# Kernel optimization log

Measured on AMD Instinct MI355X. Metric: run time of the kernel, lower is better.

## Reference

```python
import jax, jax.numpy as jnp
import numpy as np

L = 3        # num_layers
B = 8192     # batch slots
H = 1024     # hidden_dim (== decoder_in_dim)
D_IN = 1024
D_OUT = 80
N_ACT = 4096 # active rows selected by hidden_idx


def setup_inputs() -> dict:
    key = jax.random.key(0)
    ks = jax.random.split(key, 8)
    encoded = jax.random.normal(ks[0], (B, D_IN), jnp.float32)
    hidden = jax.random.normal(ks[1], (L, B, H), jnp.float32)
    hidden_idx = jnp.arange(N_ACT, dtype=jnp.int32)  # unique, in-range batch indices
    s = 0.05  # small init scale for stable gate math
    w_ih = jax.random.normal(ks[2], (L, 3 * H, D_IN), jnp.float32) * s
    w_hh = jax.random.normal(ks[3], (L, 3 * H, H), jnp.float32) * s
    b_ih = jax.random.normal(ks[4], (L, 3 * H), jnp.float32) * s
    b_hh = jax.random.normal(ks[5], (L, 3 * H), jnp.float32) * s
    w_out = jax.random.normal(ks[6], (D_OUT, H), jnp.float32) * s
    b_out = jax.random.normal(ks[7], (D_OUT,), jnp.float32) * s
    return {"encoded": encoded, "hidden": hidden, "hidden_idx": hidden_idx,
            "w_ih": w_ih, "w_hh": w_hh, "b_ih": b_ih, "b_hh": b_hh,
            "w_out": w_out, "b_out": b_out}


def reference(encoded, hidden, hidden_idx, w_ih, w_hh, b_ih, b_hh, w_out, b_out):
    # Gather active rows, run stacked GRUCells, scatter back (eval mode: dropout = identity).
    x = encoded[hidden_idx]                       # [N, D_IN]
    new_hidden = []
    for i in range(L):                            # small fixed layer loop
        h_full = hidden[i]                        # [B, H]
        h = h_full[hidden_idx]                    # [N, H]
        gi = x @ w_ih[i].T + b_ih[i]              # [N, 3H] gates from input
        gh = h @ w_hh[i].T + b_hh[i]              # [N, 3H] gates from hidden
        i_r, i_z, i_n = jnp.split(gi, 3, axis=-1)
        h_r, h_z, h_n = jnp.split(gh, 3, axis=-1)
        r = jax.nn.sigmoid(i_r + h_r)
        z = jax.nn.sigmoid(i_z + h_z)
        n = jnp.tanh(i_n + r * h_n)
        h_out = (1.0 - z) * n + z * h             # torch GRUCell update
        x = h_out
        new_hidden.append(h_full.at[hidden_idx].set(h_out))
    y = jnp.tanh(x @ w_out.T + b_out)             # linear head + tanh activation
    output = jnp.zeros((B, D_OUT), y.dtype).at[hidden_idx].set(y)
    return (output, jnp.stack(new_hidden))
```

## Files before the change

kernel.cpp:

```cpp
#include <hip/hip_runtime.h>

typedef unsigned short ushort_t;
typedef unsigned int uint_t;
typedef __attribute__((ext_vector_type(8))) short bf16x8;
typedef __attribute__((ext_vector_type(4))) float f32x4;

constexpr int L_   = 3;
constexpr int B_   = 8192;
constexpr int H_   = 1024;
constexpr int DIN_ = 1024;
constexpr int DOUT_= 80;
constexpr int NACT_= 4096;
constexpr int G3_  = 3 * H_;

static __device__ __forceinline__ ushort_t f2bf(float f) {
    uint_t u = __float_as_uint(f);
    uint_t r = (u + 0x7FFFu + ((u >> 16) & 1u)) >> 16;
    return (ushort_t)r;
}

static __device__ __forceinline__ void gll16(const void* g, void* l) {
    __builtin_amdgcn_global_load_lds(
        (const __attribute__((address_space(1))) uint32_t*)g,
        (__attribute__((address_space(3))) uint32_t*)l, 16, 0, 0);
}

__global__ void prep_convert(const float* __restrict__ wih, const float* __restrict__ whh,
                             const float* __restrict__ wout,
                             ushort_t* __restrict__ oih, ushort_t* __restrict__ ohh,
                             ushort_t* __restrict__ oout) {
    int tid = blockIdx.x * blockDim.x + threadIdx.x;
    int nth = gridDim.x * blockDim.x;
    const int NW = L_ * G3_ * H_ / 4;
    for (int i = tid; i < NW; i += nth) {
        float4 a = ((const float4*)wih)[i];
        ushort4 o; o.x = f2bf(a.x); o.y = f2bf(a.y); o.z = f2bf(a.z); o.w = f2bf(a.w);
        ((ushort4*)oih)[i] = o;
        float4 b = ((const float4*)whh)[i];
        ushort4 p; p.x = f2bf(b.x); p.y = f2bf(b.y); p.z = f2bf(b.z); p.w = f2bf(b.w);
        ((ushort4*)ohh)[i] = p;
    }
    const int NO = DOUT_ * H_ / 4;
    for (int i = tid; i < NO; i += nth) {
        float4 a = ((const float4*)wout)[i];
        ushort4 o; o.x = f2bf(a.x); o.y = f2bf(a.y); o.z = f2bf(a.z); o.w = f2bf(a.w);
        ((ushort4*)oout)[i] = o;
    }
}

__global__ void prep_gather(const float* __restrict__ encoded, const float* __restrict__ hidden,
                            const int* __restrict__ idx,
                            ushort_t* __restrict__ x0, ushort_t* __restrict__ hb) {
    const int C4 = H_ / 4;
    const int PER = NACT_ * C4;
    int tid = blockIdx.x * blockDim.x + threadIdx.x;
    int nth = gridDim.x * blockDim.x;
    int total = 4 * PER;
    for (int i = tid; i < total; i += nth) {
        int seg = i / PER;
        int rem = i - seg * PER;
        int r = rem / C4, c = rem % C4;
        int gr = idx[r];
        const float* src = (seg == 0) ? (encoded + (size_t)gr * DIN_)
                                      : (hidden + ((size_t)(seg - 1) * B_ + gr) * H_);
        float4 v = ((const float4*)src)[c];
        ushort4 o; o.x = f2bf(v.x); o.y = f2bf(v.y); o.z = f2bf(v.z); o.w = f2bf(v.w);
        ushort_t* dst = (seg == 0) ? x0 : (hb + (size_t)(seg - 1) * NACT_ * H_);
        ((ushort4*)(dst + (size_t)r * H_))[c] = o;
    }
}

__global__ __launch_bounds__(256, 2) void gru_layer(
    const ushort_t* __restrict__ xb,
    const ushort_t* __restrict__ hb,
    const float* __restrict__ hid_full,
    const ushort_t* __restrict__ wih,
    const ushort_t* __restrict__ whh,
    const float* __restrict__ bih, const float* __restrict__ bhh,
    const int* __restrict__ idx,
    float* __restrict__ out_hid,
    ushort_t* __restrict__ xnext)
{
    __shared__ ushort_t As[128 * 64];
    __shared__ ushort_t Ws[192 * 64];

    const int tid = threadIdx.x;
    const int bid = blockIdx.x;
    const int swz = (bid & 7) * 64 + (bid >> 3);
    const int bn = swz & 15, bm = swz >> 4;
    const int row0 = bm * 128, col0 = bn * 64;
    const int wave = tid >> 6, lane = tid & 63;
    const int wr = wave >> 1, wc = wave & 1;
    const int fl = lane & 15, fh = lane >> 4;
    const int srow = lane >> 3;
    const int sxor = ((lane & 7) ^ srow) * 8;

    f32x4 accR[4][2] = {};
    f32x4 accZ[4][2] = {};
    f32x4 accN[2][4][2] = {};

#pragma unroll
    for (int ph = 0; ph < 2; ++ph) {
        const ushort_t* Asrc = ph ? hb : xb;
        const ushort_t* Wsrc = ph ? whh : wih;
        const ushort_t* abase[4];
        const ushort_t* wbase[6];
#pragma unroll
        for (int t = 0; t < 4; ++t)
            abase[t] = Asrc + (size_t)(row0 + wave * 32 + t * 8 + srow) * H_ + sxor;
#pragma unroll
        for (int t = 0; t < 6; ++t) {
            const int slot = wave * 48 + t * 8 + srow;
            const int gate = slot >> 6, rowW = slot & 63;
            wbase[t] = Wsrc + (size_t)(gate * H_ + col0 + rowW) * H_ + sxor;
        }
        for (int kk = 0; kk < H_; kk += 64) {
            __syncthreads();
#pragma unroll
            for (int t = 0; t < 4; ++t)
                gll16(abase[t] + kk, &As[wave * 2048 + t * 512]);
#pragma unroll
            for (int t = 0; t < 6; ++t)
                gll16(wbase[t] + kk, &Ws[wave * 3072 + t * 512]);
            __syncthreads();
#pragma unroll
            for (int ks = 0; ks < 2; ++ks) {
                const int sl = ((ks * 4 + fh) ^ (fl & 7)) * 8;
                bf16x8 a[4];
#pragma unroll
                for (int m = 0; m < 4; ++m)
                    a[m] = *(const bf16x8*)&As[(wr * 64 + m * 16 + fl) * 64 + sl];
#pragma unroll
                for (int g = 0; g < 3; ++g) {
#pragma unroll
                    for (int n = 0; n < 2; ++n) {
                        const bf16x8 b = *(const bf16x8*)&Ws[(g * 64 + wc * 32 + n * 16 + fl) * 64 + sl];
#pragma unroll
                        for (int m = 0; m < 4; ++m) {
                            if (g == 0)
                                accR[m][n] = __builtin_amdgcn_mfma_f32_16x16x32_bf16(a[m], b, accR[m][n], 0, 0, 0);
                            else if (g == 1)
                                accZ[m][n] = __builtin_amdgcn_mfma_f32_16x16x32_bf16(a[m], b, accZ[m][n], 0, 0, 0);
                            else
                                accN[ph][m][n] = __builtin_amdgcn_mfma_f32_16x16x32_bf16(a[m], b, accN[ph][m][n], 0, 0, 0);
                        }
                    }
                }
            }
        }
    }

#pragma unroll
    for (int m = 0; m < 4; ++m) {
#pragma unroll
        for (int n = 0; n < 2; ++n) {
            const int c = col0 + wc * 32 + n * 16 + fl;
            const float br_r = bih[c] + bhh[c];
            const float br_z = bih[H_ + c] + bhh[H_ + c];
            const float bi_n = bih[2 * H_ + c];
            const float bh_n = bhh[2 * H_ + c];
#pragma unroll
            for (int j = 0; j < 4; ++j) {
                const int r = row0 + wr * 64 + m * 16 + fh * 4 + j;
                const float vr = 1.f / (1.f + expf(-(accR[m][n][j] + br_r)));
                const float vz = 1.f / (1.f + expf(-(accZ[m][n][j] + br_z)));
                const float vn = tanhf(accN[0][m][n][j] + bi_n + vr * (accN[1][m][n][j] + bh_n));
                const int gr = idx[r];
                const float h0 = hid_full[(size_t)gr * H_ + c];
                const float ho = (1.f - vz) * vn + vz * h0;
                out_hid[(size_t)gr * H_ + c] = ho;
                xnext[(size_t)r * H_ + c] = f2bf(ho);
            }
        }
    }
}

__global__ __launch_bounds__(256) void head_gemm(
    const ushort_t* __restrict__ xb, const ushort_t* __restrict__ wo,
    const float* __restrict__ bo, const int* __restrict__ idx,
    float* __restrict__ outy)
{
    __shared__ ushort_t Xs[64][72];
    __shared__ ushort_t Ws[80][72];
    const int tid = threadIdx.x;
    const int row0 = blockIdx.x * 64;
    const int lrow = tid >> 2, lseg = tid & 3;
    const int wave = tid >> 6, lane = tid & 63;
    const int fl = lane & 15, fh = lane >> 4;
    f32x4 acc[5] = {};

    for (int kk = 0; kk < H_; kk += 64) {
        __syncthreads();
        const ushort_t* xp = xb + (size_t)(row0 + lrow) * H_ + kk + lseg * 16;
        *(uint4*)&Xs[lrow][lseg * 16]     = *(const uint4*)xp;
        *(uint4*)&Xs[lrow][lseg * 16 + 8] = *(const uint4*)(xp + 8);
        for (int t = tid; t < 320; t += 256) {
            int r = t >> 2, s = t & 3;
            const ushort_t* wp = wo + (size_t)r * H_ + kk + s * 16;
            *(uint4*)&Ws[r][s * 16]     = *(const uint4*)wp;
            *(uint4*)&Ws[r][s * 16 + 8] = *(const uint4*)(wp + 8);
        }
        __syncthreads();
#pragma unroll
        for (int ks = 0; ks < 64; ks += 32) {
            bf16x8 a = *(const bf16x8*)&Xs[wave * 16 + fl][ks + fh * 8];
#pragma unroll
            for (int nf = 0; nf < 5; ++nf) {
                bf16x8 b = *(const bf16x8*)&Ws[nf * 16 + fl][ks + fh * 8];
                acc[nf] = __builtin_amdgcn_mfma_f32_16x16x32_bf16(a, b, acc[nf], 0, 0, 0);
            }
        }
    }
#pragma unroll
    for (int nf = 0; nf < 5; ++nf) {
        const int c = nf * 16 + fl;
        const float bb = bo[c];
#pragma unroll
        for (int j = 0; j < 4; ++j) {
            const int r = row0 + wave * 16 + fh * 4 + j;
            const float y = tanhf(acc[nf][j] + bb);
            outy[(size_t)idx[r] * DOUT_ + c] = y;
        }
    }
}

extern "C" void kernel_launch(void* const* d_in, const int* in_sizes, int n_in,
                              void* d_out, int out_size, void* d_ws, size_t ws_size,
                              hipStream_t stream) {
    const float* encoded = (const float*)d_in[0];
    const float* hidden  = (const float*)d_in[1];
    const int*   idx     = (const int*)d_in[2];
    const float* w_ih    = (const float*)d_in[3];
    const float* w_hh    = (const float*)d_in[4];
    const float* b_ih    = (const float*)d_in[5];
    const float* b_hh    = (const float*)d_in[6];
    const float* w_out   = (const float*)d_in[7];
    const float* b_out   = (const float*)d_in[8];

    float* outy = (float*)d_out;
    float* outh = outy + (size_t)B_ * DOUT_;

    ushort_t* ws    = (ushort_t*)d_ws;
    ushort_t* wihb  = ws;
    ushort_t* whhb  = wihb + (size_t)L_ * G3_ * H_;
    ushort_t* woutb = whhb + (size_t)L_ * G3_ * H_;
    ushort_t* xb0   = woutb + (size_t)DOUT_ * H_;
    ushort_t* xb1   = xb0 + (size_t)NACT_ * H_;
    ushort_t* hb    = xb1 + (size_t)NACT_ * H_;

    hipMemsetAsync(outy, 0, (size_t)B_ * DOUT_ * sizeof(float), stream);
    hipMemcpyAsync(outh, hidden, (size_t)L_ * B_ * H_ * sizeof(float),
                   hipMemcpyDeviceToDevice, stream);

    prep_convert<<<2048, 256, 0, stream>>>(w_ih, w_hh, w_out, wihb, whhb, woutb);
    prep_gather<<<2048, 256, 0, stream>>>(encoded, hidden, idx, xb0, hb);

    ushort_t* xin = xb0;
    ushort_t* xout = xb1;
    for (int i = 0; i < L_; ++i) {
        gru_layer<<<512, 256, 0, stream>>>(
            xin, hb + (size_t)i * NACT_ * H_, hidden + (size_t)i * B_ * H_,
            wihb + (size_t)i * G3_ * H_, whhb + (size_t)i * G3_ * H_,
            b_ih + (size_t)i * G3_, b_hh + (size_t)i * G3_, idx,
            outh + (size_t)i * B_ * H_, xout);
        ushort_t* t = xin; xin = xout; xout = t;
    }
    head_gemm<<<64, 256, 0, stream>>>(xin, woutb, b_out, idx, outy);
}
```

Before: 289.1 us.

## Use 32x32 MFMA tiles, fuse prep kernels, copy only inactive hidden rows

Switches the GRU layer GEMM from 16x16x32 to 32x32x16 bf16 MFMA, which cuts LDS fragment reads per MFMA. The two prep kernels are merged into one launch that also builds a mask of active rows. The full device-to-device hidden-state copy is replaced by a masked copy inside each layer kernel, so only inactive rows are copied. This removes redundant writes of active rows and one launch, at the cost of a mask memset and a byte lookup per copied element.

Measured after the change: 324.3 us. 12.2% more time.

```diff
diff --git a/kernel.cpp b/kernel.cpp
--- a/kernel.cpp
+++ b/kernel.cpp
@@ -1,14 +1,14 @@
 #include <hip/hip_runtime.h>
 
 typedef unsigned short ushort_t;
+typedef unsigned char uchar_t;
 typedef unsigned int uint_t;
 typedef __attribute__((ext_vector_type(8))) short bf16x8;
-typedef __attribute__((ext_vector_type(4))) float f32x4;
+typedef __attribute__((ext_vector_type(16))) float f32x16;
 
 constexpr int L_   = 3;
 constexpr int B_   = 8192;
 constexpr int H_   = 1024;
-constexpr int DIN_ = 1024;
 constexpr int DOUT_= 80;
 constexpr int NACT_= 4096;
 constexpr int G3_  = 3 * H_;
@@ -25,12 +25,19 @@
         (__attribute__((address_space(3))) uint32_t*)l, 16, 0, 0);
 }
 
-__global__ void prep_convert(const float* __restrict__ wih, const float* __restrict__ whh,
-                             const float* __restrict__ wout,
-                             ushort_t* __restrict__ oih, ushort_t* __restrict__ ohh,
-                             ushort_t* __restrict__ oout) {
+#define MFMA32(A, B, C) __builtin_amdgcn_mfma_f32_32x32x16_bf16((A), (B), (C), 0, 0, 0)
+
+__global__ void prep_all(const float* __restrict__ encoded, const float* __restrict__ hidden,
+                         const int* __restrict__ idx,
+                         const float* __restrict__ wih, const float* __restrict__ whh,
+                         const float* __restrict__ wout,
+                         ushort_t* __restrict__ oih, ushort_t* __restrict__ ohh,
+                         ushort_t* __restrict__ oout,
+                         ushort_t* __restrict__ x0, ushort_t* __restrict__ hb,
+                         uchar_t* __restrict__ mask) {
     int tid = blockIdx.x * blockDim.x + threadIdx.x;
     int nth = gridDim.x * blockDim.x;
+    if (tid < NACT_) mask[idx[tid]] = 1;
     const int NW = L_ * G3_ * H_ / 4;
     for (int i = tid; i < NW; i += nth) {
         float4 a = ((const float4*)wih)[i];
@@ -46,22 +53,14 @@
         ushort4 o; o.x = f2bf(a.x); o.y = f2bf(a.y); o.z = f2bf(a.z); o.w = f2bf(a.w);
         ((ushort4*)oout)[i] = o;
     }
-}
-
-__global__ void prep_gather(const float* __restrict__ encoded, const float* __restrict__ hidden,
-                            const int* __restrict__ idx,
-                            ushort_t* __restrict__ x0, ushort_t* __restrict__ hb) {
     const int C4 = H_ / 4;
     const int PER = NACT_ * C4;
-    int tid = blockIdx.x * blockDim.x + threadIdx.x;
-    int nth = gridDim.x * blockDim.x;
-    int total = 4 * PER;
-    for (int i = tid; i < total; i += nth) {
+    for (int i = tid; i < 4 * PER; i += nth) {
         int seg = i / PER;
         int rem = i - seg * PER;
         int r = rem / C4, c = rem % C4;
         int gr = idx[r];
-        const float* src = (seg == 0) ? (encoded + (size_t)gr * DIN_)
+        const float* src = (seg == 0) ? (encoded + (size_t)gr * H_)
                                       : (hidden + ((size_t)(seg - 1) * B_ + gr) * H_);
         float4 v = ((const float4*)src)[c];
         ushort4 o; o.x = f2bf(v.x); o.y = f2bf(v.y); o.z = f2bf(v.z); o.w = f2bf(v.w);
@@ -79,7 +78,8 @@
     const float* __restrict__ bih, const float* __restrict__ bhh,
     const int* __restrict__ idx,
     float* __restrict__ out_hid,
-    ushort_t* __restrict__ xnext)
+    ushort_t* __restrict__ xnext,
+    const uchar_t* __restrict__ mask)
 {
     __shared__ ushort_t As[128 * 64];
     __shared__ ushort_t Ws[192 * 64];
@@ -91,87 +91,75 @@
     const int row0 = bm * 128, col0 = bn * 64;
     const int wave = tid >> 6, lane = tid & 63;
     const int wr = wave >> 1, wc = wave & 1;
-    const int fl = lane & 15, fh = lane >> 4;
-    const int srow = lane >> 3;
-    const int sxor = ((lane & 7) ^ srow) * 8;
-
-    f32x4 accR[4][2] = {};
-    f32x4 accZ[4][2] = {};
-    f32x4 accN[2][4][2] = {};
+    const int l5 = lane & 31, hk = lane >> 5;
+    const int sr = lane >> 3, ss = (lane & 7) ^ sr;
+
+    f32x16 accR[2] = {}, accZ[2] = {}, accN[2][2] = {};
 
 #pragma unroll
     for (int ph = 0; ph < 2; ++ph) {
         const ushort_t* Asrc = ph ? hb : xb;
         const ushort_t* Wsrc = ph ? whh : wih;
-        const ushort_t* abase[4];
-        const ushort_t* wbase[6];
+        const ushort_t* ab[4];
+        const ushort_t* wb[6];
 #pragma unroll
         for (int t = 0; t < 4; ++t)
-            abase[t] = Asrc + (size_t)(row0 + wave * 32 + t * 8 + srow) * H_ + sxor;
+            ab[t] = Asrc + (size_t)(row0 + wave * 32 + t * 8 + sr) * H_ + ss * 8;
 #pragma unroll
         for (int t = 0; t < 6; ++t) {
-            const int slot = wave * 48 + t * 8 + srow;
-            const int gate = slot >> 6, rowW = slot & 63;
-            wbase[t] = Wsrc + (size_t)(gate * H_ + col0 + rowW) * H_ + sxor;
+            const int fr = wave * 48 + t * 8 + sr;
+            wb[t] = Wsrc + (size_t)((fr >> 6) * H_ + col0 + (fr & 63)) * H_ + ss * 8;
         }
         for (int kk = 0; kk < H_; kk += 64) {
             __syncthreads();
 #pragma unroll
-            for (int t = 0; t < 4; ++t)
-                gll16(abase[t] + kk, &As[wave * 2048 + t * 512]);
-#pragma unroll
-            for (int t = 0; t < 6; ++t)
-                gll16(wbase[t] + kk, &Ws[wave * 3072 + t * 512]);
+            for (int t = 0; t < 4; ++t) gll16(ab[t] + kk, &As[(wave * 32 + t * 8) * 64]);
+#pragma unroll
+            for (int t = 0; t < 6; ++t) gll16(wb[t] + kk, &Ws[(wave * 48 + t * 8) * 64]);
             __syncthreads();
 #pragma unroll
-            for (int ks = 0; ks < 2; ++ks) {
-                const int sl = ((ks * 4 + fh) ^ (fl & 7)) * 8;
-                bf16x8 a[4];
-#pragma unroll
-                for (int m = 0; m < 4; ++m)
-                    a[m] = *(const bf16x8*)&As[(wr * 64 + m * 16 + fl) * 64 + sl];
-#pragma unroll
-                for (int g = 0; g < 3; ++g) {
-#pragma unroll
-                    for (int n = 0; n < 2; ++n) {
-                        const bf16x8 b = *(const bf16x8*)&Ws[(g * 64 + wc * 32 + n * 16 + fl) * 64 + sl];
-#pragma unroll
-                        for (int m = 0; m < 4; ++m) {
-                            if (g == 0)
-                                accR[m][n] = __builtin_amdgcn_mfma_f32_16x16x32_bf16(a[m], b, accR[m][n], 0, 0, 0);
-                            else if (g == 1)
-                                accZ[m][n] = __builtin_amdgcn_mfma_f32_16x16x32_bf16(a[m], b, accZ[m][n], 0, 0, 0);
-                            else
-                                accN[ph][m][n] = __builtin_amdgcn_mfma_f32_16x16x32_bf16(a[m], b, accN[ph][m][n], 0, 0, 0);
-                        }
-                    }
-                }
+            for (int s = 0; s < 4; ++s) {
+                const int sl = (((s * 2 + hk) ^ (lane & 7)) << 3);
+                const bf16x8 a0 = *(const bf16x8*)&As[((wr * 64 + l5) << 6) + sl];
+                const bf16x8 a1 = *(const bf16x8*)&As[((wr * 64 + 32 + l5) << 6) + sl];
+                const bf16x8 b0 = *(const bf16x8*)&Ws[((wc * 32 + l5) << 6) + sl];
+                const bf16x8 b1 = *(const bf16x8*)&Ws[((64 + wc * 32 + l5) << 6) + sl];
+                const bf16x8 b2 = *(const bf16x8*)&Ws[((128 + wc * 32 + l5) << 6) + sl];
+                accR[0] = MFMA32(a0, b0, accR[0]);
+                accR[1] = MFMA32(a1, b0, accR[1]);
+                accZ[0] = MFMA32(a0, b1, accZ[0]);
+                accZ[1] = MFMA32(a1, b1, accZ[1]);
+                accN[ph][0] = MFMA32(a0, b2, accN[ph][0]);
+                accN[ph][1] = MFMA32(a1, b2, accN[ph][1]);
             }
         }
     }
 
-#pragma unroll
-    for (int m = 0; m < 4; ++m) {
-#pragma unroll
-        for (int n = 0; n < 2; ++n) {
-            const int c = col0 + wc * 32 + n * 16 + fl;
-            const float br_r = bih[c] + bhh[c];
-            const float br_z = bih[H_ + c] + bhh[H_ + c];
-            const float bi_n = bih[2 * H_ + c];
-            const float bh_n = bhh[2 * H_ + c];
-#pragma unroll
-            for (int j = 0; j < 4; ++j) {
-                const int r = row0 + wr * 64 + m * 16 + fh * 4 + j;
-                const float vr = 1.f / (1.f + expf(-(accR[m][n][j] + br_r)));
-                const float vz = 1.f / (1.f + expf(-(accZ[m][n][j] + br_z)));
-                const float vn = tanhf(accN[0][m][n][j] + bi_n + vr * (accN[1][m][n][j] + bh_n));
-                const int gr = idx[r];
-                const float h0 = hid_full[(size_t)gr * H_ + c];
-                const float ho = (1.f - vz) * vn + vz * h0;
-                out_hid[(size_t)gr * H_ + c] = ho;
-                xnext[(size_t)r * H_ + c] = f2bf(ho);
-            }
-        }
+    const int c = col0 + wc * 32 + l5;
+    const float br_r = bih[c] + bhh[c];
+    const float br_z = bih[H_ + c] + bhh[H_ + c];
+    const float bi_n = bih[2 * H_ + c];
+    const float bh_n = bhh[2 * H_ + c];
+#pragma unroll
+    for (int mf = 0; mf < 2; ++mf) {
+#pragma unroll
+        for (int reg = 0; reg < 16; ++reg) {
+            const int r = row0 + wr * 64 + mf * 32 + (reg & 3) + ((reg >> 2) << 3) + (hk << 2);
+            const float vr = 1.f / (1.f + expf(-(accR[mf][reg] + br_r)));
+            const float vz = 1.f / (1.f + expf(-(accZ[mf][reg] + br_z)));
+            const float vn = tanhf(accN[0][mf][reg] + bi_n + vr * (accN[1][mf][reg] + bh_n));
+            const int gr = idx[r];
+            const float h0 = hid_full[(size_t)gr * H_ + c];
+            const float ho = (1.f - vz) * vn + vz * h0;
+            out_hid[(size_t)gr * H_ + c] = ho;
+            xnext[(size_t)r * H_ + c] = f2bf(ho);
+        }
+    }
+
+    const int tot = B_ * (H_ / 4);
+    for (int i = bid * 256 + tid; i < tot; i += 512 * 256) {
+        const int row = i >> 8;
+        if (!mask[row]) ((float4*)out_hid)[i] = ((const float4*)hid_full)[i];
     }
 }
 
@@ -182,6 +170,7 @@
 {
     __shared__ ushort_t Xs[64][72];
     __shared__ ushort_t Ws[80][72];
+    typedef __attribute__((ext_vector_type(4))) float f32x4;
     const int tid = threadIdx.x;
     const int row0 = blockIdx.x * 64;
     const int lrow = tid >> 2, lseg = tid & 3;
@@ -247,13 +236,12 @@
     ushort_t* xb0   = woutb + (size_t)DOUT_ * H_;
     ushort_t* xb1   = xb0 + (size_t)NACT_ * H_;
     ushort_t* hb    = xb1 + (size_t)NACT_ * H_;
+    uchar_t*  mask  = (uchar_t*)(hb + (size_t)L_ * NACT_ * H_);
 
     hipMemsetAsync(outy, 0, (size_t)B_ * DOUT_ * sizeof(float), stream);
-    hipMemcpyAsync(outh, hidden, (size_t)L_ * B_ * H_ * sizeof(float),
-                   hipMemcpyDeviceToDevice, stream);
-
-    prep_convert<<<2048, 256, 0, stream>>>(w_ih, w_hh, w_out, wihb, whhb, woutb);
-    prep_gather<<<2048, 256, 0, stream>>>(encoded, hidden, idx, xb0, hb);
+    hipMemsetAsync(mask, 0, B_, stream);
+    prep_all<<<2048, 256, 0, stream>>>(encoded, hidden, idx, w_ih, w_hh, w_out,
+                                       wihb, whhb, woutb, xb0, hb, mask);
 
     ushort_t* xin = xb0;
     ushort_t* xout = xb1;
@@ -262,7 +250,7 @@
             xin, hb + (size_t)i * NACT_ * H_, hidden + (size_t)i * B_ * H_,
             wihb + (size_t)i * G3_ * H_, whhb + (size_t)i * G3_ * H_,
             b_ih + (size_t)i * G3_, b_hh + (size_t)i * G3_, idx,
-            outh + (size_t)i * B_ * H_, xout);
+            outh + (size_t)i * B_ * H_, xout, mask);
         ushort_t* t = xin; xin = xout; xout = t;
     }
     head_gemm<<<64, 256, 0, stream>>>(xin, woutb, b_out, idx, outy);
```

## Replace full hidden memcpy with masked copy of inactive rows in GRU kernels

Applied to the files above, without the earlier changes.

Drops the device-to-device copy of the whole hidden tensor. Each layer kernel instead copies only the rows not selected by hidden_idx, using a byte mask built in a merged prep kernel. The active rows are written by the GRU epilogue anyway, so their redundant copy traffic is avoided. The weight conversion and gather kernels are merged into one launch. This adds a tail loop and a mask lookup to the compute kernel.

Measured after the change: 300.3 us. 3.9% more time.

```diff
diff --git a/kernel.cpp b/kernel.cpp
--- a/kernel.cpp
+++ b/kernel.cpp
@@ -1,6 +1,7 @@
 #include <hip/hip_runtime.h>
 
 typedef unsigned short ushort_t;
+typedef unsigned char uchar_t;
 typedef unsigned int uint_t;
 typedef __attribute__((ext_vector_type(8))) short bf16x8;
 typedef __attribute__((ext_vector_type(4))) float f32x4;
@@ -8,7 +9,6 @@
 constexpr int L_   = 3;
 constexpr int B_   = 8192;
 constexpr int H_   = 1024;
-constexpr int DIN_ = 1024;
 constexpr int DOUT_= 80;
 constexpr int NACT_= 4096;
 constexpr int G3_  = 3 * H_;
@@ -25,12 +25,17 @@
         (__attribute__((address_space(3))) uint32_t*)l, 16, 0, 0);
 }
 
-__global__ void prep_convert(const float* __restrict__ wih, const float* __restrict__ whh,
-                             const float* __restrict__ wout,
-                             ushort_t* __restrict__ oih, ushort_t* __restrict__ ohh,
-                             ushort_t* __restrict__ oout) {
+__global__ void prep_all(const float* __restrict__ encoded, const float* __restrict__ hidden,
+                         const int* __restrict__ idx,
+                         const float* __restrict__ wih, const float* __restrict__ whh,
+                         const float* __restrict__ wout,
+                         ushort_t* __restrict__ oih, ushort_t* __restrict__ ohh,
+                         ushort_t* __restrict__ oout,
+                         ushort_t* __restrict__ x0, ushort_t* __restrict__ hb,
+                         uchar_t* __restrict__ mask) {
     int tid = blockIdx.x * blockDim.x + threadIdx.x;
     int nth = gridDim.x * blockDim.x;
+    if (tid < NACT_) mask[idx[tid]] = 1;
     const int NW = L_ * G3_ * H_ / 4;
     for (int i = tid; i < NW; i += nth) {
         float4 a = ((const float4*)wih)[i];
@@ -46,22 +51,14 @@
         ushort4 o; o.x = f2bf(a.x); o.y = f2bf(a.y); o.z = f2bf(a.z); o.w = f2bf(a.w);
         ((ushort4*)oout)[i] = o;
     }
-}
-
-__global__ void prep_gather(const float* __restrict__ encoded, const float* __restrict__ hidden,
-                            const int* __restrict__ idx,
-                            ushort_t* __restrict__ x0, ushort_t* __restrict__ hb) {
     const int C4 = H_ / 4;
     const int PER = NACT_ * C4;
-    int tid = blockIdx.x * blockDim.x + threadIdx.x;
-    int nth = gridDim.x * blockDim.x;
-    int total = 4 * PER;
-    for (int i = tid; i < total; i += nth) {
+    for (int i = tid; i < 4 * PER; i += nth) {
         int seg = i / PER;
         int rem = i - seg * PER;
         int r = rem / C4, c = rem % C4;
         int gr = idx[r];
-        const float* src = (seg == 0) ? (encoded + (size_t)gr * DIN_)
+        const float* src = (seg == 0) ? (encoded + (size_t)gr * H_)
                                       : (hidden + ((size_t)(seg - 1) * B_ + gr) * H_);
         float4 v = ((const float4*)src)[c];
         ushort4 o; o.x = f2bf(v.x); o.y = f2bf(v.y); o.z = f2bf(v.z); o.w = f2bf(v.w);
@@ -79,7 +76,8 @@
     const float* __restrict__ bih, const float* __restrict__ bhh,
     const int* __restrict__ idx,
     float* __restrict__ out_hid,
-    ushort_t* __restrict__ xnext)
+    ushort_t* __restrict__ xnext,
+    const uchar_t* __restrict__ mask)
 {
     __shared__ ushort_t As[128 * 64];
     __shared__ ushort_t Ws[192 * 64];
@@ -172,6 +170,12 @@
                 xnext[(size_t)r * H_ + c] = f2bf(ho);
             }
         }
+    }
+
+    const int tot = B_ * (H_ / 4);
+    for (int i = bid * 256 + tid; i < tot; i += 512 * 256) {
+        const int row = i >> 8;
+        if (!mask[row]) ((float4*)out_hid)[i] = ((const float4*)hid_full)[i];
     }
 }
 
@@ -247,13 +251,12 @@
     ushort_t* xb0   = woutb + (size_t)DOUT_ * H_;
     ushort_t* xb1   = xb0 + (size_t)NACT_ * H_;
     ushort_t* hb    = xb1 + (size_t)NACT_ * H_;
+    uchar_t*  mask  = (uchar_t*)(hb + (size_t)L_ * NACT_ * H_);
 
     hipMemsetAsync(outy, 0, (size_t)B_ * DOUT_ * sizeof(float), stream);
-    hipMemcpyAsync(outh, hidden, (size_t)L_ * B_ * H_ * sizeof(float),
-                   hipMemcpyDeviceToDevice, stream);
-
-    prep_convert<<<2048, 256, 0, stream>>>(w_ih, w_hh, w_out, wihb, whhb, woutb);
-    prep_gather<<<2048, 256, 0, stream>>>(encoded, hidden, idx, xb0, hb);
+    hipMemsetAsync(mask, 0, B_, stream);
+    prep_all<<<2048, 256, 0, stream>>>(encoded, hidden, idx, w_ih, w_hh, w_out,
+                                       wihb, whhb, woutb, xb0, hb, mask);
 
     ushort_t* xin = xb0;
     ushort_t* xout = xb1;
@@ -262,7 +265,7 @@
             xin, hb + (size_t)i * NACT_ * H_, hidden + (size_t)i * B_ * H_,
             wihb + (size_t)i * G3_ * H_, whhb + (size_t)i * G3_ * H_,
             b_ih + (size_t)i * G3_, b_hh + (size_t)i * G3_, idx,
-            outh + (size_t)i * B_ * H_, xout);
+            outh + (size_t)i * B_ * H_, xout, mask);
         ushort_t* t = xin; xin = xout; xout = t;
     }
     head_gemm<<<64, 256, 0, stream>>>(xin, woutb, b_out, idx, outy);
```
